# Optimization experiments

Measured on AMD Instinct MI355X. Metric: run time of the kernel, lower is better.

## Reference

```python
import jax, jax.numpy as jnp
import numpy as np

EPS = 1e-5


def _batchnorm(x, gamma, beta):
    # training-mode BatchNorm over the point/voxel dim (axis 0)
    mean = jnp.mean(x, axis=0)
    var = jnp.var(x, axis=0)
    return (x - mean) * jax.lax.rsqrt(var + EPS) * gamma + beta


def setup_inputs() -> dict:
    N, P, NI, NF, K, I = 100000, 200000, 32, 64, 27, 8
    key = jax.random.key(0)
    ks = jax.random.split(key, 10)
    return {
        "x_feats": jax.random.normal(ks[0], (N, NI), jnp.float32),
        "z_feats": jax.random.normal(ks[1], (P, NI), jnp.float32),
        "interp_w": jax.random.uniform(ks[2], (P, I), jnp.float32),
        "nbr_idx": jax.random.randint(ks[3], (N, K), 0, N, jnp.int32),
        "interp_idx": jax.random.randint(ks[4], (P, I), 0, N, jnp.int32),
        "p2v_idx": jax.random.randint(ks[5], (P,), 0, N, jnp.int32),
        "conv1_w": jax.random.normal(ks[6], (K, NI, NF), jnp.float32) / np.float32(np.sqrt(K * NI)),
        "conv2_w": jax.random.normal(ks[7], (K, NF, NF), jnp.float32) / np.float32(np.sqrt(K * NF)),
        "bn_gamma": jnp.ones((NF,), jnp.float32),
        "bn_beta": jnp.zeros((NF,), jnp.float32),
        "pbn_gamma": jnp.ones((NI,), jnp.float32),
        "pbn_beta": jnp.zeros((NI,), jnp.float32),
        "lin_w": jax.random.normal(ks[8], (NI, NF), jnp.float32) / np.float32(np.sqrt(NI)),
        "lin_b": jnp.zeros((NF,), jnp.float32),
    }


def reference(x_feats, z_feats, interp_w, nbr_idx, interp_idx, p2v_idx,
              conv1_w, conv2_w, bn_gamma, bn_beta, pbn_gamma, pbn_beta,
              lin_w, lin_b):
    N = x_feats.shape[0]
    # --- voxel branch: Conv3d -> BN -> SiLU -> Conv3d (submanifold sparse conv
    # = neighbor gather via kernel map + grouped GEMM over 27 offsets) ---
    h = jnp.einsum('nki,kio->no', x_feats[nbr_idx], conv1_w)   # [N, NF]
    h = jax.nn.silu(_batchnorm(h, bn_gamma, bn_beta))
    x = jnp.einsum('nki,kio->no', h[nbr_idx], conv2_w)         # [N, NF]
    # --- voxel_to_point: trilinear gather from 8 surrounding voxels ---
    z1 = jnp.sum(x[interp_idx] * interp_w[..., None], axis=1)  # [P, NF]
    # --- point branch: z1.F += Linear(SiLU(BN(z.F))) ---
    pz = jax.nn.silu(_batchnorm(z_feats, pbn_gamma, pbn_beta))
    z1 = z1 + pz @ lin_w + lin_b                               # [P, NF]
    # --- point_to_voxel: scatter-average point features into voxels ---
    sums = jax.ops.segment_sum(z1, p2v_idx, num_segments=N)    # [N, NF]
    cnt = jax.ops.segment_sum(jnp.ones((z1.shape[0], 1), z1.dtype), p2v_idx,
                              num_segments=N)
    x_new = sums / jnp.maximum(cnt, 1.0)
    return (x_new, z1)
```

## Files before the change

### kernel.cpp

```cpp
#include <hip/hip_runtime.h>
#include <cstdint>

#define EPSF 1e-5f
constexpr int KOFF = 27;

typedef __attribute__((ext_vector_type(8))) short bf16x8;
typedef __attribute__((ext_vector_type(4))) float f32x4;
typedef unsigned short ushort_t;
typedef unsigned int uint_t;

__device__ __forceinline__ ushort_t f2b(float f) {
    uint_t u = __float_as_uint(f);
    u += 0x7fffu + ((u >> 16) & 1u);
    return (ushort_t)(u >> 16);
}
__device__ __forceinline__ void u4tof(uint4 u, float* f) {
    uint_t w[4] = {u.x, u.y, u.z, u.w};
#pragma unroll
    for (int i = 0; i < 4; ++i) {
        f[2 * i]     = __uint_as_float(w[i] << 16);
        f[2 * i + 1] = __uint_as_float(w[i] & 0xffff0000u);
    }
}

__device__ __forceinline__ void gload_lds16(const void* g, float* l) {
    __builtin_amdgcn_global_load_lds(
        (const __attribute__((address_space(1))) void*)g,
        (__attribute__((address_space(3))) void*)l, 16, 0, 0);
}

__global__ __launch_bounds__(256) void cvt_k(const float* __restrict__ in,
                                             ushort_t* __restrict__ out, int n8) {
    int i = blockIdx.x * 256 + threadIdx.x;
    if (i >= n8) return;
    float4 a = ((const float4*)in)[2 * i];
    float4 b = ((const float4*)in)[2 * i + 1];
    uint4 o;
    o.x = (uint_t)f2b(a.x) | ((uint_t)f2b(a.y) << 16);
    o.y = (uint_t)f2b(a.z) | ((uint_t)f2b(a.w) << 16);
    o.z = (uint_t)f2b(b.x) | ((uint_t)f2b(b.y) << 16);
    o.w = (uint_t)f2b(b.z) | ((uint_t)f2b(b.w) << 16);
    ((uint4*)out)[i] = o;
}

__global__ __launch_bounds__(256) void wtT_k(const float* __restrict__ W,
                                             ushort_t* __restrict__ Wt, int CIN) {
    int t     = blockIdx.x * 256 + threadIdx.x;
    int total = KOFF * CIN * 64;
    if (t >= total) return;
    int o    = t & 63;
    int rest = t >> 6;
    int i    = rest % CIN;
    int k    = rest / CIN;
    Wt[((size_t)k * 64 + o) * CIN + i] = f2b(W[t]);
}

template <int CIN>
__global__ __launch_bounds__(256) void convm_k(
    const ushort_t* __restrict__ feats,
    const int* __restrict__ nbr,
    const ushort_t* __restrict__ Wt,
    ushort_t* __restrict__ outp,
    int N) {
    constexpr int CHUNKS = CIN / 8;
    constexpr int T      = CIN / 32;
    constexpr int NS     = CHUNKS / 4;
    constexpr int M      = CHUNKS - 1;
    constexpr int PH     = 3;
    constexpr int NPH    = KOFF / PH;

    __shared__ float lds[2][PH][64 * CHUNKS * 4];

    const int lane = threadIdx.x & 63;
    const int wv   = threadIdx.x >> 6;
    const int lo   = lane & 15;
    const int hi   = lane >> 4;
    const int row0 = blockIdx.x * 64;

    int srcoff[NS];
    const int* nbp[NS];
    int ldsbase[NS];
#pragma unroll
    for (int i = 0; i < NS; ++i) {
        int c      = (wv * NS + i) * 64 + lane;
        int r      = c / CHUNKS;
        int ch     = c & M;
        srcoff[i]  = (ch ^ (r & M)) * 8;
        int grow   = row0 + r;
        if (grow >= N) grow = N - 1;
        nbp[i]     = nbr + (size_t)grow * KOFF;
        ldsbase[i] = (wv * NS + i) * 256;
    }

    f32x4 acc[4] = {{0.f, 0.f, 0.f, 0.f},
                    {0.f, 0.f, 0.f, 0.f},
                    {0.f, 0.f, 0.f, 0.f},
                    {0.f, 0.f, 0.f, 0.f}};

    int idxb[2][PH][NS];
    bf16x8 Bb[2][PH][T];

    auto LOADIDX = [&](int pp) {
#pragma unroll
        for (int s = 0; s < PH; ++s)
#pragma unroll
            for (int i = 0; i < NS; ++i)
                idxb[pp & 1][s][i] = nbp[i][pp * PH + s];
    };
    auto LOADB = [&](int pp) {
#pragma unroll
        for (int s = 0; s < PH; ++s) {
            const ushort_t* wb =
                Wt + ((size_t)(pp * PH + s) * 64 + wv * 16 + lo) * CIN + hi * 8;
#pragma unroll
            for (int t = 0; t < T; ++t)
                Bb[pp & 1][s][t] = *(const bf16x8*)(wb + t * 32);
        }
    };
    auto STAGE = [&](int pp) {
#pragma unroll
        for (int s = 0; s < PH; ++s)
#pragma unroll
            for (int i = 0; i < NS; ++i) {
                const ushort_t* src =
                    feats + (size_t)idxb[pp & 1][s][i] * CIN + srcoff[i];
                gload_lds16(src, &lds[pp & 1][s][ldsbase[i]]);
            }
    };

    LOADIDX(0);
    LOADIDX(1);
    LOADB(0);
    STAGE(0);
    __syncthreads();

#pragma unroll
    for (int p = 0; p < NPH; ++p) {
        if (p + 2 < NPH) LOADIDX(p + 2);
        if (p + 1 < NPH) LOADB(p + 1);
        if (p + 1 < NPH) STAGE(p + 1);
        __builtin_amdgcn_sched_barrier(0);
#pragma unroll
        for (int s = 0; s < PH; ++s) {
#pragma unroll
            for (int mt = 0; mt < 4; ++mt) {
                const int R = mt * 16 + lo;
#pragma unroll
                for (int t = 0; t < T; ++t) {
                    int d    = t * 4 + hi;
                    int slot = d ^ (R & M);
                    bf16x8 a =
                        *(const bf16x8*)&lds[p & 1][s][(R * CHUNKS + slot) * 4];
                    acc[mt] = __builtin_amdgcn_mfma_f32_16x16x32_bf16(
                        a, Bb[p & 1][s][t], acc[mt], 0, 0, 0);
                }
            }
        }
        __syncthreads();
    }

#pragma unroll
    for (int mt = 0; mt < 4; ++mt) {
#pragma unroll
        for (int r = 0; r < 4; ++r) {
            int orow = row0 + mt * 16 + hi * 4 + r;
            if (orow < N)
                outp[(size_t)orow * 64 + wv * 16 + lo] = f2b(acc[mt][r]);
        }
    }
}

__global__ __launch_bounds__(256) void statsp1_k(const float* __restrict__ v,
                                                 int n, float* __restrict__ part) {
    __shared__ float ls[2 * 256];
    const int c = threadIdx.x & 31;
    int r0      = blockIdx.x * 8 + (threadIdx.x >> 5);
    int stride  = gridDim.x * 8;
    float s = 0.f, ss = 0.f;
    for (int r = r0; r < n; r += stride) {
        float x = v[(size_t)r * 32 + c];
        s += x;
        ss += x * x;
    }
    ls[threadIdx.x]       = s;
    ls[256 + threadIdx.x] = ss;
    __syncthreads();
    for (int off = 128; off >= 32; off >>= 1) {
        if (threadIdx.x < off) {
            ls[threadIdx.x] += ls[threadIdx.x + off];
            ls[256 + threadIdx.x] += ls[256 + threadIdx.x + off];
        }
        __syncthreads();
    }
    if (threadIdx.x < 32) {
        part[(size_t)blockIdx.x * 64 + threadIdx.x]      = ls[threadIdx.x];
        part[(size_t)blockIdx.x * 64 + 32 + threadIdx.x] = ls[256 + threadIdx.x];
    }
}

__global__ __launch_bounds__(256) void statsb1_k(const ushort_t* __restrict__ v,
                                                 int n, float* __restrict__ part) {
    __shared__ float ls[2][256];
    const int c8 = threadIdx.x & 7;
    int r0 = blockIdx.x * 32 + (threadIdx.x >> 3);
    float s[8], ss[8];
#pragma unroll
    for (int j = 0; j < 8; ++j) { s[j] = 0.f; ss[j] = 0.f; }
    for (int r = r0; r < n; r += gridDim.x * 32) {
        uint4 u = *(const uint4*)(v + (size_t)r * 64 + c8 * 8);
        float f[8];
        u4tof(u, f);
#pragma unroll
        for (int j = 0; j < 8; ++j) { s[j] += f[j]; ss[j] += f[j] * f[j]; }
    }
#pragma unroll
    for (int j = 0; j < 8; ++j) {
        ls[0][threadIdx.x] = s[j];
        ls[1][threadIdx.x] = ss[j];
        __syncthreads();
        for (int off = 128; off >= 8; off >>= 1) {
            if (threadIdx.x < off) {
                ls[0][threadIdx.x] += ls[0][threadIdx.x + off];
                ls[1][threadIdx.x] += ls[1][threadIdx.x + off];
            }
            __syncthreads();
        }
        if (threadIdx.x < 8) {
            part[(size_t)blockIdx.x * 128 + threadIdx.x * 8 + j]      = ls[0][threadIdx.x];
            part[(size_t)blockIdx.x * 128 + 64 + threadIdx.x * 8 + j] = ls[1][threadIdx.x];
        }
        __syncthreads();
    }
}

__global__ __launch_bounds__(128) void statsr_k(const float* __restrict__ part,
                                                float* __restrict__ out,
                                                int G, int C2) {
    int c = threadIdx.x;
    if (c >= C2) return;
    float s = 0.f;
#pragma unroll 8
    for (int g = 0; g < G; ++g) s += part[(size_t)g * C2 + c];
    out[c] = s;
}

__global__ __launch_bounds__(256) void bnsilub_k(ushort_t* __restrict__ h,
                                                 const float* __restrict__ stats,
                                                 const float* __restrict__ gamma,
                                                 const float* __restrict__ beta,
                                                 int total8, float invN) {
    int i8 = blockIdx.x * 256 + threadIdx.x;
    if (i8 >= total8) return;
    int c0  = (i8 * 8) & 63;
    uint4 u = ((const uint4*)h)[i8];
    float f[8];
    u4tof(u, f);
#pragma unroll
    for (int j = 0; j < 8; ++j) {
        int c     = c0 + j;
        float m   = stats[c] * invN;
        float var = stats[64 + c] * invN - m * m;
        float x   = (f[j] - m) * rsqrtf(var + EPSF) * gamma[c] + beta[c];
        f[j]      = x / (1.f + expf(-x));
    }
    uint4 o;
    o.x = (uint_t)f2b(f[0]) | ((uint_t)f2b(f[1]) << 16);
    o.y = (uint_t)f2b(f[2]) | ((uint_t)f2b(f[3]) << 16);
    o.z = (uint_t)f2b(f[4]) | ((uint_t)f2b(f[5]) << 16);
    o.w = (uint_t)f2b(f[6]) | ((uint_t)f2b(f[7]) << 16);
    ((uint4*)h)[i8] = o;
}

__global__ __launch_bounds__(256) void point_k(
    const ushort_t* __restrict__ x,
    const float* __restrict__ z_feats, const float* __restrict__ interp_w,
    const int* __restrict__ interp_idx, const float* __restrict__ lin_w,
    const float* __restrict__ lin_b, const float* __restrict__ pstats,
    const float* __restrict__ pgamma, const float* __restrict__ pbeta,
    float* __restrict__ z1_out, int P, float invP) {
    const int lane = threadIdx.x & 63;
    const int wv   = threadIdx.x >> 6;
    const int p    = blockIdx.x * 64 + lane;
    if (p >= P) return;
    const int wbase = __builtin_amdgcn_readfirstlane(wv * 16);

    const int4* iip   = (const int4*)(interp_idx + (size_t)p * 8);
    const float4* iwp = (const float4*)(interp_w + (size_t)p * 8);
    int4 ia = iip[0], ib = iip[1];
    float4 wa = iwp[0], wb = iwp[1];
    int idxs[8]  = {ia.x, ia.y, ia.z, ia.w, ib.x, ib.y, ib.z, ib.w};
    float wts[8] = {wa.x, wa.y, wa.z, wa.w, wb.x, wb.y, wb.z, wb.w};

    float acc[16];
#pragma unroll
    for (int o = 0; o < 16; ++o) acc[o] = 0.f;

#pragma unroll
    for (int t = 0; t < 8; ++t) {
        const ushort_t* xr = x + (size_t)idxs[t] * 64 + wbase;
        float w            = wts[t];
        uint4 u0 = *(const uint4*)xr;
        uint4 u1 = *(const uint4*)(xr + 8);
        float f[16];
        u4tof(u0, f);
        u4tof(u1, f + 8);
#pragma unroll
        for (int o = 0; o < 16; ++o) acc[o] = fmaf(w, f[o], acc[o]);
    }

    const float4* zr4 = (const float4*)(z_feats + (size_t)p * 32);
#pragma unroll
    for (int i4 = 0; i4 < 8; ++i4) {
        float4 zv = zr4[i4];
#pragma unroll
        for (int j = 0; j < 4; ++j) {
            int i     = i4 * 4 + j;
            float m   = pstats[i] * invP;
            float var = pstats[32 + i] * invP - m * m;
            float zn  = ((&zv.x)[j] - m) * rsqrtf(var + EPSF) * pgamma[i] + pbeta[i];
            float pz  = zn / (1.f + expf(-zn));
            const float* lw = lin_w + i * 64 + wbase;
#pragma unroll
            for (int o = 0; o < 16; ++o) acc[o] = fmaf(pz, lw[o], acc[o]);
        }
    }
    const float* lb = lin_b + wbase;
#pragma unroll
    for (int o = 0; o < 16; ++o) acc[o] += lb[o];

    float* zo = z1_out + (size_t)p * 64 + wbase;
#pragma unroll
    for (int o = 0; o < 16; o += 4) {
        float4 v = {acc[o], acc[o + 1], acc[o + 2], acc[o + 3]};
        *(float4*)(zo + o) = v;
    }
}

__global__ __launch_bounds__(256) void hist_k(const int* __restrict__ p2v,
                                              int* __restrict__ cnt, int P) {
    int p = blockIdx.x * 256 + threadIdx.x;
    if (p < P) atomicAdd(&cnt[p2v[p]], 1);
}

__global__ __launch_bounds__(256) void scan1_k(const int* __restrict__ cnt,
                                               int* __restrict__ tmp,
                                               int* __restrict__ bsum, int n) {
    __shared__ int s[256];
    int i = blockIdx.x * 256 + threadIdx.x;
    int v = (i < n) ? cnt[i] : 0;
    s[threadIdx.x] = v;
    __syncthreads();
    for (int off = 1; off < 256; off <<= 1) {
        int t = (threadIdx.x >= off) ? s[threadIdx.x - off] : 0;
        __syncthreads();
        s[threadIdx.x] += t;
        __syncthreads();
    }
    if (i < n) tmp[i] = s[threadIdx.x];
    if (threadIdx.x == 255) bsum[blockIdx.x] = s[255];
}

__global__ void scan2_k(const int* __restrict__ bsum, int* __restrict__ bpre,
                        int nb) {
    if (blockIdx.x == 0 && threadIdx.x == 0) {
        int a = 0;
        for (int b = 0; b < nb; ++b) { bpre[b] = a; a += bsum[b]; }
    }
}

__global__ __launch_bounds__(256) void scan3_k(const int* __restrict__ cnt,
                                               const int* __restrict__ tmp,
                                               const int* __restrict__ bpre,
                                               int* __restrict__ off, int n) {
    int i = blockIdx.x * 256 + threadIdx.x;
    if (i < n) off[i] = bpre[i >> 8] + tmp[i] - cnt[i];
}

__global__ __launch_bounds__(256) void fill_k(const int* __restrict__ p2v,
                                              const int* __restrict__ off,
                                              int* __restrict__ cursor,
                                              int* __restrict__ bucket, int P) {
    int p = blockIdx.x * 256 + threadIdx.x;
    if (p >= P) return;
    int v    = p2v[p];
    int slot = atomicAdd(&cursor[v], 1);
    bucket[off[v] + slot] = p;
}

__global__ __launch_bounds__(256) void avg_k(const float* __restrict__ z1,
                                             const int* __restrict__ off,
                                             const int* __restrict__ cnt,
                                             const int* __restrict__ bucket,
                                             float* __restrict__ xnew, int N) {
    int tid = blockIdx.x * 256 + threadIdx.x;
    int v   = tid >> 2;
    if (v >= N) return;
    int q  = tid & 3;
    int c  = cnt[v];
    int st = off[v];
    float acc[16];
#pragma unroll
    for (int o = 0; o < 16; ++o) acc[o] = 0.f;
    for (int j = 0; j < c; ++j) {
        int p            = bucket[st + j];
        const float4* zr = (const float4*)(z1 + (size_t)p * 64 + q * 16);
#pragma unroll
        for (int c4 = 0; c4 < 4; ++c4) {
            float4 t = zr[c4];
            acc[c4 * 4 + 0] += t.x;
            acc[c4 * 4 + 1] += t.y;
            acc[c4 * 4 + 2] += t.z;
            acc[c4 * 4 + 3] += t.w;
        }
    }
    float rc  = 1.f / fmaxf((float)c, 1.f);
    float* op = xnew + (size_t)v * 64 + q * 16;
#pragma unroll
    for (int o = 0; o < 16; o += 4) {
        float4 t = {acc[o] * rc, acc[o + 1] * rc, acc[o + 2] * rc, acc[o + 3] * rc};
        *(float4*)(op + o) = t;
    }
}

extern "C" void kernel_launch(void* const* d_in, const int* in_sizes, int n_in,
                              void* d_out, int out_size, void* d_ws, size_t ws_size,
                              hipStream_t stream) {
    const float* x_feats   = (const float*)d_in[0];
    const float* z_feats   = (const float*)d_in[1];
    const float* interp_w  = (const float*)d_in[2];
    const int* nbr_idx     = (const int*)d_in[3];
    const int* interp_idx  = (const int*)d_in[4];
    const int* p2v_idx     = (const int*)d_in[5];
    const float* conv1_w   = (const float*)d_in[6];
    const float* conv2_w   = (const float*)d_in[7];
    const float* bn_gamma  = (const float*)d_in[8];
    const float* bn_beta   = (const float*)d_in[9];
    const float* pbn_gamma = (const float*)d_in[10];
    const float* pbn_beta  = (const float*)d_in[11];
    const float* lin_w     = (const float*)d_in[12];
    const float* lin_b     = (const float*)d_in[13];

    const int N  = in_sizes[3] / KOFF;
    const int P  = in_sizes[5];
    const int NB = (N + 255) / 256;
    const int GH = 512;
    const int GP = 256;

    ushort_t* h2   = (ushort_t*)d_ws;
    ushort_t* xb   = h2 + (size_t)N * 64;
    ushort_t* xf16 = xb + (size_t)N * 64;
    ushort_t* wt1  = xf16 + (size_t)N * 32;
    ushort_t* wt2  = wt1 + KOFF * 64 * 32;
    int* cnt       = (int*)(wt2 + KOFF * 64 * 64);
    int* cursor    = cnt + N;
    float* stats   = (float*)(cursor + N);
    int* tmp       = (int*)(stats + 192);
    int* off       = tmp + N;
    int* bsum      = off + N;
    int* bpre      = bsum + 512;
    int* bucket    = bpre + 512;
    float* part_h  = (float*)(bucket + P);
    float* part_p  = part_h + (size_t)GH * 128;
    float* stats_h = stats;
    float* stats_p = stats + 128;

    float* xnew = (float*)d_out;
    float* z1   = xnew + (size_t)N * 64;

    hipMemsetAsync(cnt, 0, (size_t)2 * N * sizeof(int), stream);

    cvt_k<<<((size_t)N * 32 / 8 + 255) / 256, 256, 0, stream>>>(x_feats, xf16,
                                                                N * 32 / 8);
    wtT_k<<<(KOFF * 32 * 64 + 255) / 256, 256, 0, stream>>>(conv1_w, wt1, 32);
    wtT_k<<<(KOFF * 64 * 64 + 255) / 256, 256, 0, stream>>>(conv2_w, wt2, 64);

    hist_k<<<(P + 255) / 256, 256, 0, stream>>>(p2v_idx, cnt, P);
    scan1_k<<<NB, 256, 0, stream>>>(cnt, tmp, bsum, N);
    scan2_k<<<1, 1, 0, stream>>>(bsum, bpre, NB);
    scan3_k<<<NB, 256, 0, stream>>>(cnt, tmp, bpre, off, N);
    fill_k<<<(P + 255) / 256, 256, 0, stream>>>(p2v_idx, off, cursor, bucket, P);

    statsp1_k<<<GP, 256, 0, stream>>>(z_feats, P, part_p);
    statsr_k<<<1, 128, 0, stream>>>(part_p, stats_p, GP, 64);

    convm_k<32><<<(N + 63) / 64, 256, 0, stream>>>(xf16, nbr_idx, wt1, h2, N);

    statsb1_k<<<GH, 256, 0, stream>>>(h2, N, part_h);
    statsr_k<<<1, 128, 0, stream>>>(part_h, stats_h, GH, 128);
    bnsilub_k<<<((size_t)N * 64 / 8 + 255) / 256, 256, 0, stream>>>(
        h2, stats_h, bn_gamma, bn_beta, N * 64 / 8, 1.f / (float)N);

    convm_k<64><<<(N + 63) / 64, 256, 0, stream>>>(h2, nbr_idx, wt2, xb, N);

    point_k<<<(P + 63) / 64, 256, 0, stream>>>(xb, z_feats, interp_w, interp_idx,
                                               lin_w, lin_b, stats_p, pbn_gamma,
                                               pbn_beta, z1, P, 1.f / (float)P);

    avg_k<<<((size_t)N * 4 + 255) / 256, 256, 0, stream>>>(z1, off, cnt, bucket,
                                                           xnew, N);

    (void)n_in; (void)out_size; (void)ws_size;
}
```

Before: 325.3 us.

## Compute point-branch linear layer with bf16 MFMA via shared memory staging

Inside point_k, the BN+SiLU of z_feats is now computed once per point-channel cooperatively across the four waves, packed to bf16 in LDS, and multiplied by a pre-transposed bf16 lin_w using MFMA 16x16x32 instructions. The results are staged in LDS and used to initialise the accumulators, replacing the per-wave redundant scalar FMA loop where each wave recomputed all 32 normalised inputs. This removes four-fold redundant expf/normalisation work and scalar FMAs. In exchange it adds two block barriers, extra LDS traffic, a small transpose kernel, and bf16 rounding of the linear layer inputs.

```diff
diff --git a/kernel.cpp b/kernel.cpp
--- a/kernel.cpp
+++ b/kernel.cpp
@@ -55,13 +55,18 @@
     Wt[((size_t)k * 64 + o) * CIN + i] = f2b(W[t]);
 }
 
+__global__ __launch_bounds__(256) void linT_k(const float* __restrict__ lw,
+                                              ushort_t* __restrict__ wt) {
+    int t = blockIdx.x * 256 + threadIdx.x;
+    if (t >= 64 * 32) return;
+    int o = t >> 5, i = t & 31;
+    wt[o * 32 + i] = f2b(lw[i * 64 + o]);
+}
+
 template <int CIN>
 __global__ __launch_bounds__(256) void convm_k(
-    const ushort_t* __restrict__ feats,
-    const int* __restrict__ nbr,
-    const ushort_t* __restrict__ Wt,
-    ushort_t* __restrict__ outp,
-    int N) {
+    const ushort_t* __restrict__ feats, const int* __restrict__ nbr,
+    const ushort_t* __restrict__ Wt, ushort_t* __restrict__ outp, int N) {
     constexpr int CHUNKS = CIN / 8;
     constexpr int T      = CIN / 32;
     constexpr int NS     = CHUNKS / 4;
@@ -273,14 +278,69 @@
 
 __global__ __launch_bounds__(256) void point_k(
     const ushort_t* __restrict__ x,
-    const float* __restrict__ z_feats, const float* __restrict__ interp_w,
-    const int* __restrict__ interp_idx, const float* __restrict__ lin_w,
-    const float* __restrict__ lin_b, const float* __restrict__ pstats,
-    const float* __restrict__ pgamma, const float* __restrict__ pbeta,
-    float* __restrict__ z1_out, int P, float invP) {
+    const float* __restrict__ z_feats,
+    const float* __restrict__ interp_w,
+    const int* __restrict__ interp_idx,
+    const ushort_t* __restrict__ lin_wt,
+    const float* __restrict__ lin_b,
+    const float* __restrict__ pstats, const float* __restrict__ pgamma,
+    const float* __restrict__ pbeta, float* __restrict__ z1_out,
+    int P, float invP) {
+    __shared__ ushort_t pz[64 * 40];
+    __shared__ float zl[64 * 68];
+
     const int lane = threadIdx.x & 63;
     const int wv   = threadIdx.x >> 6;
-    const int p    = blockIdx.x * 64 + lane;
+    const int lo   = lane & 15;
+    const int hi   = lane >> 4;
+    const int p0   = blockIdx.x * 64;
+
+    {
+        int pp = p0 + lane;
+        if (pp >= P) pp = P - 1;
+        const int cb      = wv;
+        const float4* zr  = (const float4*)(z_feats + (size_t)pp * 32 + cb * 8);
+        float4 z0 = zr[0], z1v = zr[1];
+        float f[8] = {z0.x, z0.y, z0.z, z0.w, z1v.x, z1v.y, z1v.z, z1v.w};
+        uint_t pk[4];
+#pragma unroll
+        for (int j2 = 0; j2 < 4; ++j2) {
+            ushort_t lo16, hi16;
+#pragma unroll
+            for (int e = 0; e < 2; ++e) {
+                int j     = j2 * 2 + e;
+                int c     = cb * 8 + j;
+                float m   = pstats[c] * invP;
+                float var = pstats[32 + c] * invP - m * m;
+                float zn  = (f[j] - m) * rsqrtf(var + EPSF) * pgamma[c] + pbeta[c];
+                float pzv = zn / (1.f + expf(-zn));
+                ushort_t b = f2b(pzv);
+                if (e == 0) lo16 = b; else hi16 = b;
+            }
+            pk[j2] = (uint_t)lo16 | ((uint_t)hi16 << 16);
+        }
+        *(uint4*)&pz[lane * 40 + cb * 8] = make_uint4(pk[0], pk[1], pk[2], pk[3]);
+    }
+    __syncthreads();
+
+    {
+        bf16x8 a = *(const bf16x8*)&pz[(wv * 16 + lo) * 40 + hi * 8];
+        f32x4 lacc[4];
+#pragma unroll
+        for (int nt = 0; nt < 4; ++nt) {
+            bf16x8 b = *(const bf16x8*)(lin_wt + (size_t)(nt * 16 + lo) * 32 + hi * 8);
+            lacc[nt] = __builtin_amdgcn_mfma_f32_16x16x32_bf16(
+                a, b, (f32x4){0.f, 0.f, 0.f, 0.f}, 0, 0, 0);
+        }
+#pragma unroll
+        for (int nt = 0; nt < 4; ++nt)
+#pragma unroll
+            for (int r = 0; r < 4; ++r)
+                zl[(wv * 16 + hi * 4 + r) * 68 + nt * 16 + lo] = lacc[nt][r];
+    }
+    __syncthreads();
+
+    const int p = p0 + lane;
     if (p >= P) return;
     const int wbase = __builtin_amdgcn_readfirstlane(wv * 16);
 
@@ -293,7 +353,11 @@
 
     float acc[16];
 #pragma unroll
-    for (int o = 0; o < 16; ++o) acc[o] = 0.f;
+    for (int o4 = 0; o4 < 4; ++o4) {
+        f32x4 lv = *(const f32x4*)&zl[lane * 68 + wbase + o4 * 4];
+#pragma unroll
+        for (int j = 0; j < 4; ++j) acc[o4 * 4 + j] = lv[j];
+    }
 
 #pragma unroll
     for (int t = 0; t < 8; ++t) {
@@ -308,22 +372,6 @@
         for (int o = 0; o < 16; ++o) acc[o] = fmaf(w, f[o], acc[o]);
     }
 
-    const float4* zr4 = (const float4*)(z_feats + (size_t)p * 32);
-#pragma unroll
-    for (int i4 = 0; i4 < 8; ++i4) {
-        float4 zv = zr4[i4];
-#pragma unroll
-        for (int j = 0; j < 4; ++j) {
-            int i     = i4 * 4 + j;
-            float m   = pstats[i] * invP;
-            float var = pstats[32 + i] * invP - m * m;
-            float zn  = ((&zv.x)[j] - m) * rsqrtf(var + EPSF) * pgamma[i] + pbeta[i];
-            float pz  = zn / (1.f + expf(-zn));
-            const float* lw = lin_w + i * 64 + wbase;
-#pragma unroll
-            for (int o = 0; o < 16; ++o) acc[o] = fmaf(pz, lw[o], acc[o]);
-        }
-    }
     const float* lb = lin_b + wbase;
 #pragma unroll
     for (int o = 0; o < 16; ++o) acc[o] += lb[o];
@@ -446,23 +494,24 @@
     const int GH = 512;
     const int GP = 256;
 
-    ushort_t* h2   = (ushort_t*)d_ws;
-    ushort_t* xb   = h2 + (size_t)N * 64;
-    ushort_t* xf16 = xb + (size_t)N * 64;
-    ushort_t* wt1  = xf16 + (size_t)N * 32;
-    ushort_t* wt2  = wt1 + KOFF * 64 * 32;
-    int* cnt       = (int*)(wt2 + KOFF * 64 * 64);
-    int* cursor    = cnt + N;
-    float* stats   = (float*)(cursor + N);
-    int* tmp       = (int*)(stats + 192);
-    int* off       = tmp + N;
-    int* bsum      = off + N;
-    int* bpre      = bsum + 512;
-    int* bucket    = bpre + 512;
-    float* part_h  = (float*)(bucket + P);
-    float* part_p  = part_h + (size_t)GH * 128;
-    float* stats_h = stats;
-    float* stats_p = stats + 128;
+    ushort_t* h2    = (ushort_t*)d_ws;
+    ushort_t* xb    = h2 + (size_t)N * 64;
+    ushort_t* xf16  = xb + (size_t)N * 64;
+    ushort_t* wt1   = xf16 + (size_t)N * 32;
+    ushort_t* wt2   = wt1 + KOFF * 64 * 32;
+    ushort_t* lwt   = wt2 + KOFF * 64 * 64;
+    int* cnt        = (int*)(lwt + 64 * 32);
+    int* cursor     = cnt + N;
+    float* stats    = (float*)(cursor + N);
+    int* tmp        = (int*)(stats + 192);
+    int* off        = tmp + N;
+    int* bsum       = off + N;
+    int* bpre       = bsum + 512;
+    int* bucket     = bpre + 512;
+    float* part_h   = (float*)(bucket + P);
+    float* part_p   = part_h + (size_t)GH * 128;
+    float* stats_h  = stats;
+    float* stats_p  = stats + 128;
 
     float* xnew = (float*)d_out;
     float* z1   = xnew + (size_t)N * 64;
@@ -473,6 +522,7 @@
                                                                 N * 32 / 8);
     wtT_k<<<(KOFF * 32 * 64 + 255) / 256, 256, 0, stream>>>(conv1_w, wt1, 32);
     wtT_k<<<(KOFF * 64 * 64 + 255) / 256, 256, 0, stream>>>(conv2_w, wt2, 64);
+    linT_k<<<8, 256, 0, stream>>>(lin_w, lwt);
 
     hist_k<<<(P + 255) / 256, 256, 0, stream>>>(p2v_idx, cnt, P);
     scan1_k<<<NB, 256, 0, stream>>>(cnt, tmp, bsum, N);
@@ -493,7 +543,7 @@
     convm_k<64><<<(N + 63) / 64, 256, 0, stream>>>(h2, nbr_idx, wt2, xb, N);
 
     point_k<<<(P + 63) / 64, 256, 0, stream>>>(xb, z_feats, interp_w, interp_idx,
-                                               lin_w, lin_b, stats_p, pbn_gamma,
+                                               lwt, lin_b, stats_p, pbn_gamma,
                                                pbn_beta, z1, P, 1.f / (float)P);
 
     avg_k<<<((size_t)N * 4 + 255) / 256, 256, 0, stream>>>(z1, off, cnt, bucket,
```

Result: faster. 316.3 us (-2.8%).
